# Optimization experiments

Hardware: AMD Instinct MI355X
Metric: run time of the kernel (lower is better)

Reference implementation:

```python
import jax, jax.numpy as jnp
import numpy as np

B, D, H = 524288, 256, 4
DH = D // H
LN_EPS = 1e-5


def setup_inputs() -> dict:
    key = jax.random.key(0)
    ks = jax.random.split(key, 3)
    s = 0.02  # typical init scale
    return {
        "x": jax.random.normal(ks[0], (B, 2, D), dtype=jnp.float32),
        "in_proj_w": jax.random.normal(ks[1], (3 * D, D), dtype=jnp.float32) * s,
        "in_proj_b": jnp.zeros((3 * D,), dtype=jnp.float32),
        "out_proj_w": jax.random.normal(ks[2], (D, D), dtype=jnp.float32) * s,
        "out_proj_b": jnp.zeros((D,), dtype=jnp.float32),
        "ln_gamma": jnp.ones((D,), dtype=jnp.float32),
        "ln_beta": jnp.zeros((D,), dtype=jnp.float32),
    }


def _mha_1to1(q, k, v, Wq, bq, Wk, bk, Wv, bv, Wo, bo):
    # q, k, v: [B, D]  (seq_len == 1 collapsed). Faithful MHA math.
    Q = (q @ Wq.T + bq).reshape(-1, H, DH)  # [B,H,DH]
    K = (k @ Wk.T + bk).reshape(-1, H, DH)
    V = (v @ Wv.T + bv).reshape(-1, H, DH)
    scores = jnp.sum(Q * K, axis=-1, keepdims=True) / np.sqrt(DH)  # [B,H,1]
    w = jax.nn.softmax(scores, axis=-1)  # softmax over a single key -> 1
    out = (w * V).reshape(-1, D)  # [B,D]
    return out @ Wo.T + bo


def reference(x, in_proj_w, in_proj_b, out_proj_w, out_proj_b, ln_gamma, ln_beta):
    Wq, Wk, Wv = jnp.split(in_proj_w, 3, axis=0)
    bq, bk, bv = jnp.split(in_proj_b, 3, axis=0)
    x0, x1 = x[:, 0, :], x[:, 1, :]
    out12 = _mha_1to1(x0, x1, x1, Wq, bq, Wk, bk, Wv, bv, out_proj_w, out_proj_b)
    out21 = _mha_1to1(x1, x0, x0, Wq, bq, Wk, bk, Wv, bv, out_proj_w, out_proj_b)
    fused = jnp.stack([out12, out21], axis=1)  # [B,2,D]
    y = x + fused  # dropout = identity in eval
    mu = jnp.mean(y, axis=-1, keepdims=True)
    var = jnp.var(y, axis=-1, keepdims=True)
    return (y - mu) * jax.lax.rsqrt(var + LN_EPS) * ln_gamma + ln_beta
```

## Files before the change

kernel.cpp:

```cpp
#include <hip/hip_runtime.h>

#define DD 256
#define TOTROWS (524288 * 2)
#define NBLOCKS 256
#define RPI 64
#define ITERS (TOTROWS / (NBLOCKS * RPI))
#define XROW 528
#define XBUF(i) ((i) * (RPI * XROW))
#define YBUF(i) (2 * RPI * XROW + (i) * (RPI * XROW))
#define LDS_TOTAL (4 * RPI * XROW)

typedef __attribute__((ext_vector_type(8))) short short8;
typedef __attribute__((ext_vector_type(4))) float f32x4;
typedef __attribute__((ext_vector_type(4))) unsigned short u16x4;

__device__ inline unsigned short f2bf(float x) {
    unsigned u = __builtin_bit_cast(unsigned, x);
    u += 0x7fffu + ((u >> 16) & 1u);
    return (unsigned short)(u >> 16);
}
__device__ inline float bf2f(unsigned short h) {
    unsigned u = ((unsigned)h) << 16;
    return __builtin_bit_cast(float, u);
}

__device__ inline void block_sync_lds() {
    __builtin_amdgcn_sched_barrier(0);
    asm volatile("s_waitcnt lgkmcnt(0)" ::: "memory");
    __builtin_amdgcn_s_barrier();
    __builtin_amdgcn_sched_barrier(0);
}

__global__ void wprep_kernel(const float* __restrict__ in_w,
                             const float* __restrict__ in_b,
                             const float* __restrict__ out_w,
                             const float* __restrict__ out_b,
                             unsigned short* __restrict__ Wbf,
                             float* __restrict__ cvec) {
    __shared__ float worow[DD];
    __shared__ float part[DD];
    const int i = blockIdx.x;
    const int j = threadIdx.x;
    worow[j] = out_w[i * DD + j];
    __syncthreads();
    const float* wv = in_w + 512 * DD;
    float s = 0.f;
    for (int k = 0; k < DD; ++k) s = fmaf(worow[k], wv[k * DD + j], s);
    Wbf[i * DD + j] = f2bf(s);
    part[j] = worow[j] * in_b[512 + j];
    __syncthreads();
    if (j == 0) {
        float c = out_b[i];
        for (int k = 0; k < DD; ++k) c += part[k];
        cvec[i] = c;
    }
}

__global__ __launch_bounds__(512, 2) void fused_kernel(
    const float* __restrict__ x, const unsigned short* __restrict__ Wbf,
    const float* __restrict__ cvec, const float* __restrict__ gamma,
    const float* __restrict__ beta, float* __restrict__ out) {
    extern __shared__ __align__(16) char lds[];
    const int tid = threadIdx.x;
    const int w = tid >> 6, lane = tid & 63;
    const int m = lane & 15, g = lane >> 4;
    const int lc = lane & 7, lr = lane >> 3;

    short8 af[2][8];
#pragma unroll
    for (int n2 = 0; n2 < 2; ++n2)
#pragma unroll
        for (int s = 0; s < 8; ++s)
            af[n2][s] = *(const short8*)(Wbf + (w * 32 + n2 * 16 + m) * 256 + s * 32 + g * 8);

    f32x4 creg[2];
#pragma unroll
    for (int n2 = 0; n2 < 2; ++n2)
        creg[n2] = *(const f32x4*)(cvec + w * 32 + n2 * 16 + g * 4);
    f32x4 gg[8], bb[8];
#pragma unroll
    for (int k = 0; k < 8; ++k) {
        gg[k] = *(const f32x4*)(gamma + lc * 4 + k * 32);
        bb[k] = *(const f32x4*)(beta + lc * 4 + k * 32);
    }

    const size_t rowbase = (size_t)blockIdx.x * (ITERS * RPI);

    f32x4 sv[8];
#pragma unroll
    for (int j = 0; j < 8; ++j)
        sv[j] = *(const f32x4*)(x + rowbase * DD + j * 2048 + tid * 4);
#pragma unroll
    for (int j = 0; j < 8; ++j) {
        const int row = j * 8 + w;
        u16x4 h = {f2bf(sv[j][0]), f2bf(sv[j][1]), f2bf(sv[j][2]), f2bf(sv[j][3])};
        *(u16x4*)(lds + XBUF(0) + row * XROW + lane * 8) = h;
    }
#pragma unroll
    for (int j = 0; j < 8; ++j)
        sv[j] = *(const f32x4*)(x + (rowbase + RPI) * DD + j * 2048 + tid * 4);
    block_sync_lds();

    for (int it = 0; it < ITERS; ++it) {
        const int xbc = XBUF(it & 1);
        const int xbn = XBUF((it + 1) & 1);
        const int ybA = YBUF(it & 1);
        const int ybB = YBUF((it + 1) & 1);
        const size_t r0 = rowbase + (size_t)it * RPI;

        if (it > 0) {
            const size_t rp = r0 - RPI + w * 8 + lr;
            u16x4 yh[8];
#pragma unroll
            for (int k = 0; k < 8; ++k)
                yh[k] = *(const u16x4*)(lds + ybB + (w * 8 + lr) * XROW + lc * 8 + k * 64);
            float s1 = 0.f, s2 = 0.f;
            float f[8][4];
#pragma unroll
            for (int k = 0; k < 8; ++k)
#pragma unroll
                for (int e = 0; e < 4; ++e) {
                    float v = bf2f(yh[k][e]);
                    f[k][e] = v;
                    s1 += v;
                    s2 = fmaf(v, v, s2);
                }
            s1 += __shfl_xor(s1, 1); s2 += __shfl_xor(s2, 1);
            s1 += __shfl_xor(s1, 2); s2 += __shfl_xor(s2, 2);
            s1 += __shfl_xor(s1, 4); s2 += __shfl_xor(s2, 4);
            const float mu = s1 * (1.f / 256.f);
            const float var = s2 * (1.f / 256.f) - mu * mu;
            const float rs = rsqrtf(var + 1e-5f);
#pragma unroll
            for (int k = 0; k < 8; ++k) {
                f32x4 o;
#pragma unroll
                for (int e = 0; e < 4; ++e)
                    o[e] = fmaf((f[k][e] - mu) * rs, gg[k][e], bb[k][e]);
                __builtin_nontemporal_store(o, (f32x4*)(out + rp * DD + lc * 4 + k * 32));
            }
        }

        f32x4 acc[4][2];
#pragma unroll
        for (int t = 0; t < 4; ++t) {
            acc[t][0] = f32x4{0.f, 0.f, 0.f, 0.f};
            acc[t][1] = f32x4{0.f, 0.f, 0.f, 0.f};
        }
#pragma unroll
        for (int t = 0; t < 4; ++t) {
            const int rowp = t * 16 + (m ^ 1);
            const char* bbase = lds + xbc + rowp * XROW + g * 16;
#pragma unroll
            for (int s = 0; s < 8; ++s) {
                short8 bf_ = *(const short8*)(bbase + s * 64);
                acc[t][0] = __builtin_amdgcn_mfma_f32_16x16x32_bf16(af[0][s], bf_, acc[t][0], 0, 0, 0);
                acc[t][1] = __builtin_amdgcn_mfma_f32_16x16x32_bf16(af[1][s], bf_, acc[t][1], 0, 0, 0);
            }
        }
#pragma unroll
        for (int t = 0; t < 4; ++t) {
            const int rowm = t * 16 + m;
#pragma unroll
            for (int n2 = 0; n2 < 2; ++n2) {
                u16x4 rh = *(const u16x4*)(lds + xbc + rowm * XROW + w * 64 + n2 * 32 + g * 8);
                f32x4 y = acc[t][n2];
#pragma unroll
                for (int i = 0; i < 4; ++i) y[i] += bf2f(rh[i]) + creg[n2][i];
                u16x4 hy = {f2bf(y[0]), f2bf(y[1]), f2bf(y[2]), f2bf(y[3])};
                *(u16x4*)(lds + ybA + rowm * XROW + w * 64 + n2 * 32 + g * 8) = hy;
            }
        }

        if (it + 1 < ITERS) {
#pragma unroll
            for (int j = 0; j < 8; ++j) {
                const int row = j * 8 + w;
                u16x4 h = {f2bf(sv[j][0]), f2bf(sv[j][1]), f2bf(sv[j][2]), f2bf(sv[j][3])};
                *(u16x4*)(lds + xbn + row * XROW + lane * 8) = h;
            }
        }
        if (it + 2 < ITERS) {
#pragma unroll
            for (int j = 0; j < 8; ++j)
                sv[j] = *(const f32x4*)(x + (r0 + 2 * RPI) * DD + j * 2048 + tid * 4);
        }
        block_sync_lds();
    }

    {
        const int ybB = YBUF((ITERS - 1) & 1);
        const size_t rp = rowbase + (size_t)(ITERS - 1) * RPI + w * 8 + lr;
        u16x4 yh[8];
#pragma unroll
        for (int k = 0; k < 8; ++k)
            yh[k] = *(const u16x4*)(lds + ybB + (w * 8 + lr) * XROW + lc * 8 + k * 64);
        float s1 = 0.f, s2 = 0.f;
        float f[8][4];
#pragma unroll
        for (int k = 0; k < 8; ++k)
#pragma unroll
            for (int e = 0; e < 4; ++e) {
                float v = bf2f(yh[k][e]);
                f[k][e] = v;
                s1 += v;
                s2 = fmaf(v, v, s2);
            }
        s1 += __shfl_xor(s1, 1); s2 += __shfl_xor(s2, 1);
        s1 += __shfl_xor(s1, 2); s2 += __shfl_xor(s2, 2);
        s1 += __shfl_xor(s1, 4); s2 += __shfl_xor(s2, 4);
        const float mu = s1 * (1.f / 256.f);
        const float var = s2 * (1.f / 256.f) - mu * mu;
        const float rs = rsqrtf(var + 1e-5f);
#pragma unroll
        for (int k = 0; k < 8; ++k) {
            f32x4 o;
#pragma unroll
            for (int e = 0; e < 4; ++e)
                o[e] = fmaf((f[k][e] - mu) * rs, gg[k][e], bb[k][e]);
            __builtin_nontemporal_store(o, (f32x4*)(out + rp * DD + lc * 4 + k * 32));
        }
    }
}

extern "C" void kernel_launch(void* const* d_in, const int* in_sizes, int n_in,
                              void* d_out, int out_size, void* d_ws, size_t ws_size,
                              hipStream_t stream) {
    const float* x     = (const float*)d_in[0];
    const float* in_w  = (const float*)d_in[1];
    const float* in_b  = (const float*)d_in[2];
    const float* out_w = (const float*)d_in[3];
    const float* out_b = (const float*)d_in[4];
    const float* gamma = (const float*)d_in[5];
    const float* beta  = (const float*)d_in[6];
    float* out = (float*)d_out;

    unsigned short* Wbf = (unsigned short*)d_ws;
    float* cvec = (float*)((char*)d_ws + 131072);

    hipLaunchKernelGGL(wprep_kernel, dim3(256), dim3(256), 0, stream,
                       in_w, in_b, out_w, out_b, Wbf, cvec);

    hipFuncSetAttribute(reinterpret_cast<const void*>(fused_kernel),
                        hipFuncAttributeMaxDynamicSharedMemorySize, LDS_TOTAL);
    hipLaunchKernelGGL(fused_kernel, dim3(NBLOCKS), dim3(512), LDS_TOTAL, stream,
                       x, Wbf, cvec, gamma, beta, out);
}
```

Measured before the change: 420.1 us.

## Halve rows per iteration and deepen x prefetch to four LDS buffers

Cuts the per-iteration tile from 64 to 32 rows and switches from double to quadruple buffering of x in LDS. The loop is unrolled by two with ping-pong register staging, so global loads are issued three iterations ahead. The LayerNorm stage is remapped to 16 lanes per row with one more shuffle step. The aim is a deeper prefetch with fewer live registers per stage, at the cost of more barriers per row processed.

```diff
diff --git a/kernel.cpp b/kernel.cpp
--- a/kernel.cpp
+++ b/kernel.cpp
@@ -3,12 +3,12 @@
 #define DD 256
 #define TOTROWS (524288 * 2)
 #define NBLOCKS 256
-#define RPI 64
+#define RPI 32
 #define ITERS (TOTROWS / (NBLOCKS * RPI))
 #define XROW 528
 #define XBUF(i) ((i) * (RPI * XROW))
-#define YBUF(i) (2 * RPI * XROW + (i) * (RPI * XROW))
-#define LDS_TOTAL (4 * RPI * XROW)
+#define YBUF(i) (4 * RPI * XROW + (i) * (RPI * XROW))
+#define LDS_TOTAL (6 * RPI * XROW)
 
 typedef __attribute__((ext_vector_type(8))) short short8;
 typedef __attribute__((ext_vector_type(4))) float f32x4;
@@ -64,7 +64,7 @@
     const int tid = threadIdx.x;
     const int w = tid >> 6, lane = tid & 63;
     const int m = lane & 15, g = lane >> 4;
-    const int lc = lane & 7, lr = lane >> 3;
+    const int lc = lane & 15, lr = tid >> 4;
 
     short8 af[2][8];
 #pragma unroll
@@ -77,128 +77,146 @@
 #pragma unroll
     for (int n2 = 0; n2 < 2; ++n2)
         creg[n2] = *(const f32x4*)(cvec + w * 32 + n2 * 16 + g * 4);
-    f32x4 gg[8], bb[8];
-#pragma unroll
-    for (int k = 0; k < 8; ++k) {
-        gg[k] = *(const f32x4*)(gamma + lc * 4 + k * 32);
-        bb[k] = *(const f32x4*)(beta + lc * 4 + k * 32);
+    f32x4 gg[4], bb[4];
+#pragma unroll
+    for (int k = 0; k < 4; ++k) {
+        gg[k] = *(const f32x4*)(gamma + lc * 4 + k * 64);
+        bb[k] = *(const f32x4*)(beta + lc * 4 + k * 64);
     }
 
     const size_t rowbase = (size_t)blockIdx.x * (ITERS * RPI);
 
-    f32x4 sv[8];
-#pragma unroll
-    for (int j = 0; j < 8; ++j)
-        sv[j] = *(const f32x4*)(x + rowbase * DD + j * 2048 + tid * 4);
-#pragma unroll
-    for (int j = 0; j < 8; ++j) {
+    f32x4 svA[4], svB[4];
+#pragma unroll
+    for (int j = 0; j < 4; ++j)
+        svA[j] = *(const f32x4*)(x + rowbase * DD + j * 2048 + tid * 4);
+#pragma unroll
+    for (int j = 0; j < 4; ++j) {
         const int row = j * 8 + w;
-        u16x4 h = {f2bf(sv[j][0]), f2bf(sv[j][1]), f2bf(sv[j][2]), f2bf(sv[j][3])};
+        u16x4 h = {f2bf(svA[j][0]), f2bf(svA[j][1]), f2bf(svA[j][2]), f2bf(svA[j][3])};
         *(u16x4*)(lds + XBUF(0) + row * XROW + lane * 8) = h;
     }
 #pragma unroll
-    for (int j = 0; j < 8; ++j)
-        sv[j] = *(const f32x4*)(x + (rowbase + RPI) * DD + j * 2048 + tid * 4);
+    for (int j = 0; j < 4; ++j)
+        svA[j] = *(const f32x4*)(x + (rowbase + RPI) * DD + j * 2048 + tid * 4);
+#pragma unroll
+    for (int j = 0; j < 4; ++j) {
+        const int row = j * 8 + w;
+        u16x4 h = {f2bf(svA[j][0]), f2bf(svA[j][1]), f2bf(svA[j][2]), f2bf(svA[j][3])};
+        *(u16x4*)(lds + XBUF(1) + row * XROW + lane * 8) = h;
+    }
+#pragma unroll
+    for (int j = 0; j < 4; ++j)
+        svA[j] = *(const f32x4*)(x + (rowbase + 2 * RPI) * DD + j * 2048 + tid * 4);
     block_sync_lds();
 
-    for (int it = 0; it < ITERS; ++it) {
-        const int xbc = XBUF(it & 1);
-        const int xbn = XBUF((it + 1) & 1);
-        const int ybA = YBUF(it & 1);
-        const int ybB = YBUF((it + 1) & 1);
-        const size_t r0 = rowbase + (size_t)it * RPI;
-
-        if (it > 0) {
-            const size_t rp = r0 - RPI + w * 8 + lr;
-            u16x4 yh[8];
-#pragma unroll
-            for (int k = 0; k < 8; ++k)
-                yh[k] = *(const u16x4*)(lds + ybB + (w * 8 + lr) * XROW + lc * 8 + k * 64);
-            float s1 = 0.f, s2 = 0.f;
-            float f[8][4];
-#pragma unroll
-            for (int k = 0; k < 8; ++k)
-#pragma unroll
-                for (int e = 0; e < 4; ++e) {
-                    float v = bf2f(yh[k][e]);
-                    f[k][e] = v;
-                    s1 += v;
-                    s2 = fmaf(v, v, s2);
-                }
-            s1 += __shfl_xor(s1, 1); s2 += __shfl_xor(s2, 1);
-            s1 += __shfl_xor(s1, 2); s2 += __shfl_xor(s2, 2);
-            s1 += __shfl_xor(s1, 4); s2 += __shfl_xor(s2, 4);
-            const float mu = s1 * (1.f / 256.f);
-            const float var = s2 * (1.f / 256.f) - mu * mu;
-            const float rs = rsqrtf(var + 1e-5f);
-#pragma unroll
-            for (int k = 0; k < 8; ++k) {
-                f32x4 o;
-#pragma unroll
-                for (int e = 0; e < 4; ++e)
-                    o[e] = fmaf((f[k][e] - mu) * rs, gg[k][e], bb[k][e]);
-                __builtin_nontemporal_store(o, (f32x4*)(out + rp * DD + lc * 4 + k * 32));
-            }
-        }
-
-        f32x4 acc[4][2];
-#pragma unroll
-        for (int t = 0; t < 4; ++t) {
-            acc[t][0] = f32x4{0.f, 0.f, 0.f, 0.f};
-            acc[t][1] = f32x4{0.f, 0.f, 0.f, 0.f};
-        }
-#pragma unroll
-        for (int t = 0; t < 4; ++t) {
-            const int rowp = t * 16 + (m ^ 1);
-            const char* bbase = lds + xbc + rowp * XROW + g * 16;
-#pragma unroll
-            for (int s = 0; s < 8; ++s) {
-                short8 bf_ = *(const short8*)(bbase + s * 64);
-                acc[t][0] = __builtin_amdgcn_mfma_f32_16x16x32_bf16(af[0][s], bf_, acc[t][0], 0, 0, 0);
-                acc[t][1] = __builtin_amdgcn_mfma_f32_16x16x32_bf16(af[1][s], bf_, acc[t][1], 0, 0, 0);
-            }
-        }
-#pragma unroll
-        for (int t = 0; t < 4; ++t) {
-            const int rowm = t * 16 + m;
-#pragma unroll
-            for (int n2 = 0; n2 < 2; ++n2) {
-                u16x4 rh = *(const u16x4*)(lds + xbc + rowm * XROW + w * 64 + n2 * 32 + g * 8);
-                f32x4 y = acc[t][n2];
-#pragma unroll
-                for (int i = 0; i < 4; ++i) y[i] += bf2f(rh[i]) + creg[n2][i];
-                u16x4 hy = {f2bf(y[0]), f2bf(y[1]), f2bf(y[2]), f2bf(y[3])};
-                *(u16x4*)(lds + ybA + rowm * XROW + w * 64 + n2 * 32 + g * 8) = hy;
-            }
-        }
-
-        if (it + 1 < ITERS) {
-#pragma unroll
-            for (int j = 0; j < 8; ++j) {
-                const int row = j * 8 + w;
-                u16x4 h = {f2bf(sv[j][0]), f2bf(sv[j][1]), f2bf(sv[j][2]), f2bf(sv[j][3])};
-                *(u16x4*)(lds + xbn + row * XROW + lane * 8) = h;
-            }
-        }
-        if (it + 2 < ITERS) {
-#pragma unroll
-            for (int j = 0; j < 8; ++j)
-                sv[j] = *(const f32x4*)(x + (r0 + 2 * RPI) * DD + j * 2048 + tid * 4);
-        }
-        block_sync_lds();
-    }
+#define REGION(IT, SVC, SVN)                                                     \
+    {                                                                            \
+        const int it = (IT);                                                     \
+        const int xbc = XBUF(it & 3);                                            \
+        const int xbs = XBUF((it + 2) & 3);                                      \
+        const int ybA = YBUF(it & 1);                                            \
+        const int ybB = YBUF((it + 1) & 1);                                      \
+        const size_t r0 = rowbase + (size_t)it * RPI;                            \
+                                           \
+        if (it > 0) {                                                            \
+            const size_t rp = r0 - RPI + lr;                                     \
+            u16x4 yh[4];                                                         \
+            _Pragma("unroll")                                                    \
+            for (int k = 0; k < 4; ++k)                                          \
+                yh[k] = *(const u16x4*)(lds + ybB + lr * XROW + lc * 8 + k * 128);\
+            float s1 = 0.f, s2 = 0.f;                                            \
+            float f[4][4];                                                       \
+            _Pragma("unroll")                                                    \
+            for (int k = 0; k < 4; ++k)                                          \
+                _Pragma("unroll")                                                \
+                for (int e = 0; e < 4; ++e) {                                    \
+                    float v = bf2f(yh[k][e]);                                    \
+                    f[k][e] = v;                                                 \
+                    s1 += v;                                                     \
+                    s2 = fmaf(v, v, s2);                                         \
+                }                                                                \
+            s1 += __shfl_xor(s1, 1); s2 += __shfl_xor(s2, 1);                    \
+            s1 += __shfl_xor(s1, 2); s2 += __shfl_xor(s2, 2);                    \
+            s1 += __shfl_xor(s1, 4); s2 += __shfl_xor(s2, 4);                    \
+            s1 += __shfl_xor(s1, 8); s2 += __shfl_xor(s2, 8);                    \
+            const float mu = s1 * (1.f / 256.f);                                 \
+            const float var = s2 * (1.f / 256.f) - mu * mu;                      \
+            const float rs = rsqrtf(var + 1e-5f);                                \
+            _Pragma("unroll")                                                    \
+            for (int k = 0; k < 4; ++k) {                                        \
+                f32x4 o;                                                         \
+                _Pragma("unroll")                                                \
+                for (int e = 0; e < 4; ++e)                                      \
+                    o[e] = fmaf((f[k][e] - mu) * rs, gg[k][e], bb[k][e]);        \
+                __builtin_nontemporal_store(o, (f32x4*)(out + rp * DD + lc * 4 + k * 64)); \
+            }                                                                    \
+        }                                                                        \
+                        \
+        f32x4 acc[2][2];                                                         \
+        acc[0][0] = f32x4{0.f, 0.f, 0.f, 0.f};                                   \
+        acc[0][1] = f32x4{0.f, 0.f, 0.f, 0.f};                                   \
+        acc[1][0] = f32x4{0.f, 0.f, 0.f, 0.f};                                   \
+        acc[1][1] = f32x4{0.f, 0.f, 0.f, 0.f};                                   \
+        _Pragma("unroll")                                                        \
+        for (int t = 0; t < 2; ++t) {                                            \
+            const int rowp = t * 16 + (m ^ 1);                                   \
+            const char* bbase = lds + xbc + rowp * XROW + g * 16;                \
+            _Pragma("unroll")                                                    \
+            for (int s = 0; s < 8; ++s) {                                        \
+                short8 bf_ = *(const short8*)(bbase + s * 64);                   \
+                acc[t][0] = __builtin_amdgcn_mfma_f32_16x16x32_bf16(af[0][s], bf_, acc[t][0], 0, 0, 0); \
+                acc[t][1] = __builtin_amdgcn_mfma_f32_16x16x32_bf16(af[1][s], bf_, acc[t][1], 0, 0, 0); \
+            }                                                                    \
+        }                                                                        \
+        _Pragma("unroll")                                                        \
+        for (int t = 0; t < 2; ++t) {                                            \
+            const int rowm = t * 16 + m;                                         \
+            _Pragma("unroll")                                                    \
+            for (int n2 = 0; n2 < 2; ++n2) {                                     \
+                u16x4 rh = *(const u16x4*)(lds + xbc + rowm * XROW + w * 64 + n2 * 32 + g * 8); \
+                f32x4 y = acc[t][n2];                                            \
+                _Pragma("unroll")                                                \
+                for (int i = 0; i < 4; ++i) y[i] += bf2f(rh[i]) + creg[n2][i];   \
+                u16x4 hy = {f2bf(y[0]), f2bf(y[1]), f2bf(y[2]), f2bf(y[3])};     \
+                *(u16x4*)(lds + ybA + rowm * XROW + w * 64 + n2 * 32 + g * 8) = hy; \
+            }                                                                    \
+        }                                                                        \
+                                           \
+        if (it + 2 < ITERS) {                                                    \
+            _Pragma("unroll")                                                    \
+            for (int j = 0; j < 4; ++j) {                                        \
+                const int row = j * 8 + w;                                       \
+                u16x4 h = {f2bf(SVC[j][0]), f2bf(SVC[j][1]), f2bf(SVC[j][2]), f2bf(SVC[j][3])}; \
+                *(u16x4*)(lds + xbs + row * XROW + lane * 8) = h;                \
+            }                                                                    \
+        }                                                                        \
+                   \
+        if (it + 3 < ITERS) {                                                    \
+            _Pragma("unroll")                                                    \
+            for (int j = 0; j < 4; ++j)                                          \
+                SVN[j] = *(const f32x4*)(x + (r0 + 3 * RPI) * DD + j * 2048 + tid * 4); \
+        }                                                                        \
+        block_sync_lds();                                                        \
+    }
+
+    for (int itb = 0; itb < ITERS; itb += 2) {
+        REGION(itb, svA, svB);
+        REGION(itb + 1, svB, svA);
+    }
+#undef REGION
 
     {
         const int ybB = YBUF((ITERS - 1) & 1);
-        const size_t rp = rowbase + (size_t)(ITERS - 1) * RPI + w * 8 + lr;
-        u16x4 yh[8];
-#pragma unroll
-        for (int k = 0; k < 8; ++k)
-            yh[k] = *(const u16x4*)(lds + ybB + (w * 8 + lr) * XROW + lc * 8 + k * 64);
+        const size_t rp = rowbase + (size_t)(ITERS - 1) * RPI + lr;
+        u16x4 yh[4];
+#pragma unroll
+        for (int k = 0; k < 4; ++k)
+            yh[k] = *(const u16x4*)(lds + ybB + lr * XROW + lc * 8 + k * 128);
         float s1 = 0.f, s2 = 0.f;
-        float f[8][4];
-#pragma unroll
-        for (int k = 0; k < 8; ++k)
+        float f[4][4];
+#pragma unroll
+        for (int k = 0; k < 4; ++k)
 #pragma unroll
             for (int e = 0; e < 4; ++e) {
                 float v = bf2f(yh[k][e]);
@@ -209,16 +227,17 @@
         s1 += __shfl_xor(s1, 1); s2 += __shfl_xor(s2, 1);
         s1 += __shfl_xor(s1, 2); s2 += __shfl_xor(s2, 2);
         s1 += __shfl_xor(s1, 4); s2 += __shfl_xor(s2, 4);
+        s1 += __shfl_xor(s1, 8); s2 += __shfl_xor(s2, 8);
         const float mu = s1 * (1.f / 256.f);
         const float var = s2 * (1.f / 256.f) - mu * mu;
         const float rs = rsqrtf(var + 1e-5f);
 #pragma unroll
-        for (int k = 0; k < 8; ++k) {
+        for (int k = 0; k < 4; ++k) {
             f32x4 o;
 #pragma unroll
             for (int e = 0; e < 4; ++e)
                 o[e] = fmaf((f[k][e] - mu) * rs, gg[k][e], bb[k][e]);
-            __builtin_nontemporal_store(o, (f32x4*)(out + rp * DD + lc * 4 + k * 32));
+            __builtin_nontemporal_store(o, (f32x4*)(out + rp * DD + lc * 4 + k * 64));
         }
     }
 }
```

Result: no change. 419.2 us (-0.2%).

## Halve rows per iteration, double blocks, move LayerNorm params to LDS for occupancy

Applied to the files above, without the earlier changes.

Halves the rows per pipeline iteration and doubles the grid. This shrinks the LDS footprint and the per-thread register arrays (prefetch buffer, accumulators, LayerNorm temporaries), which allows launch bounds of 4 blocks per CU instead of 2. Gamma and beta move from per-thread registers into LDS, and the LayerNorm epilogue is remapped to 16 lanes per row with one extra shuffle step. The aim is higher occupancy to hide memory latency in this bandwidth-bound kernel, at the cost of more loop iterations and barriers, extra LDS reads, and possible register spills under the tighter bound.

```diff
diff --git a/kernel.cpp b/kernel.cpp
--- a/kernel.cpp
+++ b/kernel.cpp
@@ -2,13 +2,14 @@
 
 #define DD 256
 #define TOTROWS (524288 * 2)
-#define NBLOCKS 256
-#define RPI 64
+#define NBLOCKS 512
+#define RPI 32
 #define ITERS (TOTROWS / (NBLOCKS * RPI))
 #define XROW 528
 #define XBUF(i) ((i) * (RPI * XROW))
 #define YBUF(i) (2 * RPI * XROW + (i) * (RPI * XROW))
-#define LDS_TOTAL (4 * RPI * XROW)
+#define CGB (4 * RPI * XROW)
+#define LDS_TOTAL (CGB + 3 * 1024)
 
 typedef __attribute__((ext_vector_type(8))) short short8;
 typedef __attribute__((ext_vector_type(4))) float f32x4;
@@ -56,7 +57,7 @@
     }
 }
 
-__global__ __launch_bounds__(512, 2) void fused_kernel(
+__global__ __launch_bounds__(512, 4) void fused_kernel(
     const float* __restrict__ x, const unsigned short* __restrict__ Wbf,
     const float* __restrict__ cvec, const float* __restrict__ gamma,
     const float* __restrict__ beta, float* __restrict__ out) {
@@ -64,7 +65,7 @@
     const int tid = threadIdx.x;
     const int w = tid >> 6, lane = tid & 63;
     const int m = lane & 15, g = lane >> 4;
-    const int lc = lane & 7, lr = lane >> 3;
+    const int lc = lane & 15, lr = tid >> 4;
 
     short8 af[2][8];
 #pragma unroll
@@ -77,27 +78,26 @@
 #pragma unroll
     for (int n2 = 0; n2 < 2; ++n2)
         creg[n2] = *(const f32x4*)(cvec + w * 32 + n2 * 16 + g * 4);
-    f32x4 gg[8], bb[8];
-#pragma unroll
-    for (int k = 0; k < 8; ++k) {
-        gg[k] = *(const f32x4*)(gamma + lc * 4 + k * 32);
-        bb[k] = *(const f32x4*)(beta + lc * 4 + k * 32);
+
+    if (tid < 256) {
+        *(float*)(lds + CGB + 1024 + tid * 4) = gamma[tid];
+        *(float*)(lds + CGB + 2048 + tid * 4) = beta[tid];
     }
 
     const size_t rowbase = (size_t)blockIdx.x * (ITERS * RPI);
 
-    f32x4 sv[8];
-#pragma unroll
-    for (int j = 0; j < 8; ++j)
+    f32x4 sv[4];
+#pragma unroll
+    for (int j = 0; j < 4; ++j)
         sv[j] = *(const f32x4*)(x + rowbase * DD + j * 2048 + tid * 4);
 #pragma unroll
-    for (int j = 0; j < 8; ++j) {
+    for (int j = 0; j < 4; ++j) {
         const int row = j * 8 + w;
         u16x4 h = {f2bf(sv[j][0]), f2bf(sv[j][1]), f2bf(sv[j][2]), f2bf(sv[j][3])};
         *(u16x4*)(lds + XBUF(0) + row * XROW + lane * 8) = h;
     }
 #pragma unroll
-    for (int j = 0; j < 8; ++j)
+    for (int j = 0; j < 4; ++j)
         sv[j] = *(const f32x4*)(x + (rowbase + RPI) * DD + j * 2048 + tid * 4);
     block_sync_lds();
 
@@ -109,46 +109,46 @@
         const size_t r0 = rowbase + (size_t)it * RPI;
 
         if (it > 0) {
-            const size_t rp = r0 - RPI + w * 8 + lr;
-            u16x4 yh[8];
-#pragma unroll
-            for (int k = 0; k < 8; ++k)
-                yh[k] = *(const u16x4*)(lds + ybB + (w * 8 + lr) * XROW + lc * 8 + k * 64);
+            const size_t rp = r0 - RPI + lr;
+            u16x4 yh[4];
+#pragma unroll
+            for (int k = 0; k < 4; ++k)
+                yh[k] = *(const u16x4*)(lds + ybB + lr * XROW + lc * 8 + k * 128);
             float s1 = 0.f, s2 = 0.f;
-            float f[8][4];
-#pragma unroll
-            for (int k = 0; k < 8; ++k)
+#pragma unroll
+            for (int k = 0; k < 4; ++k)
 #pragma unroll
                 for (int e = 0; e < 4; ++e) {
                     float v = bf2f(yh[k][e]);
-                    f[k][e] = v;
                     s1 += v;
                     s2 = fmaf(v, v, s2);
                 }
             s1 += __shfl_xor(s1, 1); s2 += __shfl_xor(s2, 1);
             s1 += __shfl_xor(s1, 2); s2 += __shfl_xor(s2, 2);
             s1 += __shfl_xor(s1, 4); s2 += __shfl_xor(s2, 4);
+            s1 += __shfl_xor(s1, 8); s2 += __shfl_xor(s2, 8);
             const float mu = s1 * (1.f / 256.f);
             const float var = s2 * (1.f / 256.f) - mu * mu;
             const float rs = rsqrtf(var + 1e-5f);
 #pragma unroll
-            for (int k = 0; k < 8; ++k) {
+            for (int k = 0; k < 4; ++k) {
+                f32x4 gv = *(const f32x4*)(lds + CGB + 1024 + lc * 16 + k * 256);
+                f32x4 bv = *(const f32x4*)(lds + CGB + 2048 + lc * 16 + k * 256);
                 f32x4 o;
 #pragma unroll
                 for (int e = 0; e < 4; ++e)
-                    o[e] = fmaf((f[k][e] - mu) * rs, gg[k][e], bb[k][e]);
-                __builtin_nontemporal_store(o, (f32x4*)(out + rp * DD + lc * 4 + k * 32));
-            }
-        }
-
-        f32x4 acc[4][2];
-#pragma unroll
-        for (int t = 0; t < 4; ++t) {
-            acc[t][0] = f32x4{0.f, 0.f, 0.f, 0.f};
-            acc[t][1] = f32x4{0.f, 0.f, 0.f, 0.f};
-        }
-#pragma unroll
-        for (int t = 0; t < 4; ++t) {
+                    o[e] = fmaf((bf2f(yh[k][e]) - mu) * rs, gv[e], bv[e]);
+                __builtin_nontemporal_store(o, (f32x4*)(out + rp * DD + lc * 4 + k * 64));
+            }
+        }
+
+        f32x4 acc[2][2];
+        acc[0][0] = f32x4{0.f, 0.f, 0.f, 0.f};
+        acc[0][1] = f32x4{0.f, 0.f, 0.f, 0.f};
+        acc[1][0] = f32x4{0.f, 0.f, 0.f, 0.f};
+        acc[1][1] = f32x4{0.f, 0.f, 0.f, 0.f};
+#pragma unroll
+        for (int t = 0; t < 2; ++t) {
             const int rowp = t * 16 + (m ^ 1);
             const char* bbase = lds + xbc + rowp * XROW + g * 16;
 #pragma unroll
@@ -159,7 +159,7 @@
             }
         }
 #pragma unroll
-        for (int t = 0; t < 4; ++t) {
+        for (int t = 0; t < 2; ++t) {
             const int rowm = t * 16 + m;
 #pragma unroll
             for (int n2 = 0; n2 < 2; ++n2) {
@@ -174,7 +174,7 @@
 
         if (it + 1 < ITERS) {
 #pragma unroll
-            for (int j = 0; j < 8; ++j) {
+            for (int j = 0; j < 4; ++j) {
                 const int row = j * 8 + w;
                 u16x4 h = {f2bf(sv[j][0]), f2bf(sv[j][1]), f2bf(sv[j][2]), f2bf(sv[j][3])};
                 *(u16x4*)(lds + xbn + row * XROW + lane * 8) = h;
@@ -182,7 +182,7 @@
         }
         if (it + 2 < ITERS) {
 #pragma unroll
-            for (int j = 0; j < 8; ++j)
+            for (int j = 0; j < 4; ++j)
                 sv[j] = *(const f32x4*)(x + (r0 + 2 * RPI) * DD + j * 2048 + tid * 4);
         }
         block_sync_lds();
@@ -190,35 +190,36 @@
 
     {
         const int ybB = YBUF((ITERS - 1) & 1);
-        const size_t rp = rowbase + (size_t)(ITERS - 1) * RPI + w * 8 + lr;
-        u16x4 yh[8];
-#pragma unroll
-        for (int k = 0; k < 8; ++k)
-            yh[k] = *(const u16x4*)(lds + ybB + (w * 8 + lr) * XROW + lc * 8 + k * 64);
+        const size_t rp = rowbase + (size_t)(ITERS - 1) * RPI + lr;
+        u16x4 yh[4];
+#pragma unroll
+        for (int k = 0; k < 4; ++k)
+            yh[k] = *(const u16x4*)(lds + ybB + lr * XROW + lc * 8 + k * 128);
         float s1 = 0.f, s2 = 0.f;
-        float f[8][4];
-#pragma unroll
-        for (int k = 0; k < 8; ++k)
+#pragma unroll
+        for (int k = 0; k < 4; ++k)
 #pragma unroll
             for (int e = 0; e < 4; ++e) {
                 float v = bf2f(yh[k][e]);
-                f[k][e] = v;
                 s1 += v;
                 s2 = fmaf(v, v, s2);
             }
         s1 += __shfl_xor(s1, 1); s2 += __shfl_xor(s2, 1);
         s1 += __shfl_xor(s1, 2); s2 += __shfl_xor(s2, 2);
         s1 += __shfl_xor(s1, 4); s2 += __shfl_xor(s2, 4);
+        s1 += __shfl_xor(s1, 8); s2 += __shfl_xor(s2, 8);
         const float mu = s1 * (1.f / 256.f);
         const float var = s2 * (1.f / 256.f) - mu * mu;
         const float rs = rsqrtf(var + 1e-5f);
 #pragma unroll
-        for (int k = 0; k < 8; ++k) {
+        for (int k = 0; k < 4; ++k) {
+            f32x4 gv = *(const f32x4*)(lds + CGB + 1024 + lc * 16 + k * 256);
+            f32x4 bv = *(const f32x4*)(lds + CGB + 2048 + lc * 16 + k * 256);
             f32x4 o;
 #pragma unroll
             for (int e = 0; e < 4; ++e)
-                o[e] = fmaf((f[k][e] - mu) * rs, gg[k][e], bb[k][e]);
-            __builtin_nontemporal_store(o, (f32x4*)(out + rp * DD + lc * 4 + k * 32));
+                o[e] = fmaf((bf2f(yh[k][e]) - mu) * rs, gv[e], bv[e]);
+            __builtin_nontemporal_store(o, (f32x4*)(out + rp * DD + lc * 4 + k * 64));
         }
     }
 }
```

After: 690.1 us. 1.64x slower.
